# Kernel optimization log

Hardware: AMD Instinct MI355X
Metric: run time of the kernel (lower is better)

## Reference

```python
import jax, jax.numpy as jnp
import numpy as np

C = 256; HEADS = 8; LEVELS = 4; POINTS = 4; D = C // HEADS
SPATIAL = np.array([[96, 96], [48, 48], [24, 24], [12, 12]], dtype=np.int32)  # (H, W) per level
AREAS = SPATIAL[:, 0] * SPATIAL[:, 1]
HW = int(AREAS.sum())  # 12240
LSI = np.concatenate([[0], np.cumsum(AREAS)[:-1]]).astype(np.int32)
N = 1; Q = HW


def setup_inputs() -> dict:
    key = jax.random.key(0)
    ks = jax.random.split(key, 12)
    s = 0.02
    return {
        "query": jax.random.normal(ks[0], (N, Q, C), jnp.float32),
        "reference_points": jax.random.uniform(ks[1], (N, Q, LEVELS, 2), jnp.float32),
        "input_flatten": jax.random.normal(ks[2], (N, HW, C), jnp.float32),
        "input_spatial_shapes": jnp.asarray(SPATIAL),
        "input_level_start_index": jnp.asarray(LSI),
        "W_off": jax.random.normal(ks[3], (C, HEADS * LEVELS * POINTS * 2), jnp.float32) * s,
        "b_off": jax.random.normal(ks[4], (HEADS * LEVELS * POINTS * 2,), jnp.float32) * s,
        "W_attn": jax.random.normal(ks[5], (C, HEADS * LEVELS * POINTS), jnp.float32) * s,
        "b_attn": jax.random.normal(ks[6], (HEADS * LEVELS * POINTS,), jnp.float32) * s,
        "W_val": jax.random.normal(ks[7], (C, C), jnp.float32) * (1.0 / np.sqrt(C)),
        "b_val": jax.random.normal(ks[8], (C,), jnp.float32) * s,
        "W_out": jax.random.normal(ks[9], (C, C), jnp.float32) * (1.0 / np.sqrt(C)),
        "b_out": jax.random.normal(ks[10], (C,), jnp.float32) * s,
    }


def _ms_deform_attn(query, reference_points, input_flatten, sp, lsi,
                    W_off, b_off, W_attn, b_attn, W_val, b_val, W_out, b_out):
    n, q, c = query.shape
    hw = input_flatten.shape[1]
    # value projection -> [N, Hd, HW, D]
    value = (input_flatten @ W_val + b_val).reshape(n, hw, HEADS, D).transpose(0, 2, 1, 3)
    # sampling offsets [N,Q,Hd,L,P,2]
    off = (query @ W_off + b_off).reshape(n, q, HEADS, LEVELS, POINTS, 2)
    # attention weights softmaxed over L*P (done inside the fused CUDA kernel)
    attn = jax.nn.softmax((query @ W_attn + b_attn).reshape(n, q, HEADS, LEVELS * POINTS), axis=-1)
    attn = attn.reshape(n, q, HEADS, LEVELS, POINTS)
    # normalized sampling locations (reference_points last dim == 2 branch)
    norm = jnp.stack([sp[:, 1], sp[:, 0]], -1).astype(query.dtype)  # (W, H) per level
    loc = reference_points[:, :, None, :, None, :] + off / norm[None, None, None, :, None, :]
    Hl = sp[:, 0][None, None, None, :, None]
    Wl = sp[:, 1][None, None, None, :, None]
    start = lsi[None, None, None, :, None]
    # grid_sample-style (align_corners=False) pixel coordinates
    x = loc[..., 0] * Wl - 0.5
    y = loc[..., 1] * Hl - 0.5
    x0 = jnp.floor(x); y0 = jnp.floor(y)
    lx = x - x0; ly = y - y0
    x0i = x0.astype(jnp.int32); y0i = y0.astype(jnp.int32)

    def gather(yi, xi):
        valid = (xi >= 0) & (xi < Wl) & (yi >= 0) & (yi < Hl)
        idx = jnp.where(valid, start + yi * Wl + xi, 0)  # [N,Q,Hd,L,P]
        idx_t = idx.transpose(0, 2, 1, 3, 4).reshape(n, HEADS, q * LEVELS * POINTS, 1)
        g = jnp.take_along_axis(value, idx_t, axis=2)  # [N,Hd,Q*L*P,D]
        g = g.reshape(n, HEADS, q, LEVELS, POINTS, D)
        return g * valid.transpose(0, 2, 1, 3, 4)[..., None]

    def w(a):
        return a.transpose(0, 2, 1, 3, 4)[..., None]  # [N,Hd,Q,L,P,1]

    sampled = (gather(y0i, x0i) * w((1 - ly) * (1 - lx))
               + gather(y0i, x0i + 1) * w((1 - ly) * lx)
               + gather(y0i + 1, x0i) * w(ly * (1 - lx))
               + gather(y0i + 1, x0i + 1) * w(ly * lx))  # [N,Hd,Q,L,P,D]
    out = jnp.einsum('nhqlpd,nqhlp->nqhd', sampled, attn).reshape(n, q, c)
    return out @ W_out + b_out


def reference(query, reference_points, input_flatten, input_spatial_shapes, input_level_start_index,
              W_off, b_off, W_attn, b_attn, W_val, b_val, W_out, b_out):
    return _ms_deform_attn(query, reference_points, input_flatten,
                           input_spatial_shapes, input_level_start_index,
                           W_off, b_off, W_attn, b_attn, W_val, b_val, W_out, b_out)
```

## Files before the change

### kernel.cpp

```cpp
#include <hip/hip_runtime.h>

#define QTOT 12240
#define KD   256

typedef float f32x4 __attribute__((ext_vector_type(4)));
typedef short s16x8 __attribute__((ext_vector_type(8)));
typedef short s16x4 __attribute__((ext_vector_type(4)));
typedef unsigned short ushort_t;

__device__ __forceinline__ unsigned short f2b(float x) {
    union { float f; unsigned u; } c; c.f = x;
    unsigned r = c.u + 0x7fffu + ((c.u >> 16) & 1u);
    return (unsigned short)(r >> 16);
}
__device__ __forceinline__ float b2f(unsigned short u) {
    return __uint_as_float((unsigned)u << 16);
}
__device__ __forceinline__ int swz(int row, int kb) { return row * 512 + (kb ^ ((row & 7) << 4)); }

__global__ __launch_bounds__(256) void prep(
    const float* __restrict__ W_val, const float* __restrict__ W_off,
    const float* __restrict__ W_attn, const float* __restrict__ W_out,
    const float* __restrict__ b_off, const float* __restrict__ b_attn,
    ushort_t* __restrict__ WvT, ushort_t* __restrict__ WcT,
    ushort_t* __restrict__ WoT, float* __restrict__ bcomb)
{
    int id = blockIdx.x * 256 + threadIdx.x;
    if (id < 65536) { int n = id >> 8, k = id & 255; WvT[id] = f2b(W_val[k * 256 + n]); }
    else if (id < 163840) {
        int t = id - 65536; int n = t >> 8, k = t & 255;
        float v = (n < 256) ? W_off[k * 256 + n] : W_attn[k * 128 + (n - 256)];
        WcT[t] = f2b(v);
    } else if (id < 229376) {
        int t = id - 163840; int n = t >> 8, k = t & 255;
        WoT[t] = f2b(W_out[k * 256 + n]);
    } else if (id < 229760) {
        int t = id - 229376; bcomb[t] = (t < 256) ? b_off[t] : b_attn[t - 256];
    }
}

__global__ __launch_bounds__(256) void gemm1(
    const float* __restrict__ inflat, const float* __restrict__ query,
    const ushort_t* __restrict__ WvT, const ushort_t* __restrict__ WcT,
    const float* __restrict__ b_val, const float* __restrict__ bcomb,
    ushort_t* __restrict__ projb, ushort_t* __restrict__ offb,
    ushort_t* __restrict__ attnb)
{
    __shared__ char As[16384];
    const int b = blockIdx.x;
    const bool isval = b < 383;
    const int bm = (isval ? b : b - 383) * 32;
    const float* A = isval ? inflat : query;
    const ushort_t* WT = isval ? WvT : WcT;
    const int nc = isval ? 4 : 6;

    const int tid = threadIdx.x, lane = tid & 63, wave = tid >> 6;
    const int lr = lane & 15, g8 = (lane >> 4) * 8;

    {
        const float4* srcb = (const float4*)(A + (size_t)bm * KD);
        const int rem_rows = QTOT - bm;
#pragma unroll
        for (int j = 0; j < 8; ++j) {
            const int f4i = j * 256 + tid;
            const int row = f4i >> 6;
            const int colb = (f4i & 63) * 8;
            float4 f = make_float4(0.f, 0.f, 0.f, 0.f);
            if (row < rem_rows) f = srcb[f4i];
            s16x4 v;
            v[0] = f2b(f.x); v[1] = f2b(f.y); v[2] = f2b(f.z); v[3] = f2b(f.w);
            *(s16x4*)(As + swz(row, colb)) = v;
        }
    }
    __syncthreads();

    const int rg = (lane >> 4) * 4;

    for (int c = 0; c < nc; ++c) {
        const int col = c * 64 + wave * 16 + lr;
        s16x8 bfr[8];
        {
            const ushort_t* bp = WT + (size_t)col * KD + g8;
#pragma unroll
            for (int kc = 0; kc < 8; ++kc) bfr[kc] = *(const s16x8*)(bp + kc * 32);
        }
        f32x4 acc[2];
        acc[0] = (f32x4)0.f; acc[1] = (f32x4)0.f;
#pragma unroll
        for (int kc = 0; kc < 8; ++kc) {
            const int kb = (kc * 32 + g8) * 2;
            s16x8 a0 = *(const s16x8*)(As + swz(lr,      kb));
            s16x8 a1 = *(const s16x8*)(As + swz(16 + lr, kb));
            acc[0] = __builtin_amdgcn_mfma_f32_16x16x32_bf16(a0, bfr[kc], acc[0], 0, 0, 0);
            acc[1] = __builtin_amdgcn_mfma_f32_16x16x32_bf16(a1, bfr[kc], acc[1], 0, 0, 0);
        }
        const float bb = isval ? b_val[col] : bcomb[col];

        if (!isval && c >= 4) {
            const int gh = (c - 4) * 4 + wave;
            float v[2][4], m[2][4], e[2][4], s[2][4];
#pragma unroll
            for (int mf = 0; mf < 2; ++mf)
#pragma unroll
                for (int rr = 0; rr < 4; ++rr) { v[mf][rr] = acc[mf][rr] + bb; m[mf][rr] = v[mf][rr]; }
#pragma unroll
            for (int d = 1; d < 16; d <<= 1)
#pragma unroll
                for (int mf = 0; mf < 2; ++mf)
#pragma unroll
                    for (int rr = 0; rr < 4; ++rr) m[mf][rr] = fmaxf(m[mf][rr], __shfl_xor(m[mf][rr], d));
#pragma unroll
            for (int mf = 0; mf < 2; ++mf)
#pragma unroll
                for (int rr = 0; rr < 4; ++rr) { e[mf][rr] = __expf(v[mf][rr] - m[mf][rr]); s[mf][rr] = e[mf][rr]; }
#pragma unroll
            for (int d = 1; d < 16; d <<= 1)
#pragma unroll
                for (int mf = 0; mf < 2; ++mf)
#pragma unroll
                    for (int rr = 0; rr < 4; ++rr) s[mf][rr] += __shfl_xor(s[mf][rr], d);
#pragma unroll
            for (int mf = 0; mf < 2; ++mf)
#pragma unroll
                for (int rr = 0; rr < 4; ++rr) {
                    const int row = bm + mf * 16 + rg + rr;
                    if (row < QTOT)
                        attnb[(size_t)row * 128 + gh * 16 + lr] = f2b(e[mf][rr] / s[mf][rr]);
                }
        } else {
#pragma unroll
            for (int mf = 0; mf < 2; ++mf)
#pragma unroll
                for (int rr = 0; rr < 4; ++rr) {
                    const int row = bm + mf * 16 + rg + rr;
                    if (row >= QTOT) continue;
                    const float v = acc[mf][rr] + bb;
                    if (isval) projb[(size_t)row * 256 + col] = f2b(v);
                    else       offb [(size_t)row * 256 + col] = f2b(v);
                }
        }
    }
}

__global__ __launch_bounds__(256, 2) void sample7(
    const float* __restrict__ rp, const ushort_t* __restrict__ offb,
    const ushort_t* __restrict__ attnb, const ushort_t* __restrict__ projb,
    const int* __restrict__ sp, const int* __restrict__ lsi,
    ushort_t* __restrict__ outpre)
{
    const int bid = blockIdx.x;
    const int hh = (bid >= 1530) ? 1 : 0;
    const int g  = hh ? (bid - 1530) : bid;
    const int q0 = g * 8;
    const int tid = threadIdx.x;

    __shared__ int4 s_meta[512];

#pragma unroll
    for (int rep = 0; rep < 2; ++rep) {
        const int task = rep * 256 + tid;
        const int ql = task >> 6;
        const int hp = (task >> 4) & 3;
        const int lp = task & 15;
        const int l = lp >> 2;
        const int q = q0 + ql;
        const int gh = hh * 4 + hp;
        const int t128 = gh * 16 + lp;

        const float aw = b2f(attnb[(size_t)q * 128 + t128]);

        const unsigned opk = *(const unsigned*)&offb[(size_t)q * 256 + t128 * 2];
        const float ox = __uint_as_float(opk << 16);
        const float oy = __uint_as_float(opk & 0xffff0000u);

        const int Wl = 96 >> l;
        const int st = 12288 - (12288 >> (2 * l));
        const float rx = rp[((size_t)q * 4 + l) * 2 + 0];
        const float ry = rp[((size_t)q * 4 + l) * 2 + 1];

        const float x = rx * (float)Wl + ox - 0.5f;
        const float y = ry * (float)Wl + oy - 0.5f;
        const float xf = floorf(x), yf = floorf(y);
        const int x0 = (int)xf, y0 = (int)yf;
        const float lx = x - xf, ly = y - yf;

        const bool vx0 = (x0 >= 0) && (x0 < Wl);
        const bool vx1 = (x0 + 1 >= 0) && (x0 + 1 < Wl);
        const bool vy0 = (y0 >= 0) && (y0 < Wl);
        const bool vy1 = (y0 + 1 >= 0) && (y0 + 1 < Wl);

        const float w00 = (vx0 && vy0) ? aw * (1.f - ly) * (1.f - lx) : 0.f;
        const float w01 = (vx1 && vy0) ? aw * (1.f - ly) * lx         : 0.f;
        const float w10 = (vx0 && vy1) ? aw * ly * (1.f - lx)         : 0.f;
        const float w11 = (vx1 && vy1) ? aw * ly * lx                 : 0.f;
        const int i00 = (vx0 && vy0) ? st + y0 * Wl + x0           : 0;
        const int i01 = (vx1 && vy0) ? st + y0 * Wl + x0 + 1       : 0;
        const int i10 = (vx0 && vy1) ? st + (y0 + 1) * Wl + x0     : 0;
        const int i11 = (vx1 && vy1) ? st + (y0 + 1) * Wl + x0 + 1 : 0;

        int4 m;
        m.x = (i00 << 16) | (int)f2b(w00);
        m.y = (i01 << 16) | (int)f2b(w01);
        m.z = (i10 << 16) | (int)f2b(w10);
        m.w = (i11 << 16) | (int)f2b(w11);
        s_meta[task] = m;
    }
    __syncthreads();

    const int c8 = tid & 3;
    const int pq = (tid >> 2) & 1;
    const int hp = (tid >> 3) & 3;
    const int ql = tid >> 5;
    const int gh = hh * 4 + hp;
    const char* basec = (const char*)projb + (gh * 32 + c8 * 8) * 2;
    const int slot0 = (ql << 6) | (hp << 4);

    float a0 = 0, a1 = 0, a2 = 0, a3 = 0, a4 = 0, a5 = 0, a6 = 0, a7 = 0;
#pragma unroll
    for (int l = 0; l < 4; ++l) {
#pragma unroll
        for (int j = 0; j < 2; ++j) {
            const int slot = slot0 | (l << 2) | (pq * 2 + j);
            const int4 m = s_meta[slot];
#pragma unroll
            for (int c = 0; c < 4; ++c) {
                const int pk = (c == 0) ? m.x : (c == 1) ? m.y : (c == 2) ? m.z : m.w;
                const int off = (pk >> 16) << 9;
                const float w = __uint_as_float((unsigned)pk << 16);
                const uint4 v = *(const uint4*)(basec + off);
                a0 += w * __uint_as_float(v.x << 16);
                a1 += w * __uint_as_float(v.x & 0xffff0000u);
                a2 += w * __uint_as_float(v.y << 16);
                a3 += w * __uint_as_float(v.y & 0xffff0000u);
                a4 += w * __uint_as_float(v.z << 16);
                a5 += w * __uint_as_float(v.z & 0xffff0000u);
                a6 += w * __uint_as_float(v.w << 16);
                a7 += w * __uint_as_float(v.w & 0xffff0000u);
            }
        }
    }
    a0 += __shfl_xor(a0, 4); a1 += __shfl_xor(a1, 4);
    a2 += __shfl_xor(a2, 4); a3 += __shfl_xor(a3, 4);
    a4 += __shfl_xor(a4, 4); a5 += __shfl_xor(a5, 4);
    a6 += __shfl_xor(a6, 4); a7 += __shfl_xor(a7, 4);

    if (pq == 0) {
        uint4 o;
        o.x = (unsigned)f2b(a0) | ((unsigned)f2b(a1) << 16);
        o.y = (unsigned)f2b(a2) | ((unsigned)f2b(a3) << 16);
        o.z = (unsigned)f2b(a4) | ((unsigned)f2b(a5) << 16);
        o.w = (unsigned)f2b(a6) | ((unsigned)f2b(a7) << 16);
        *(uint4*)&outpre[(size_t)(q0 + ql) * 256 + gh * 32 + c8 * 8] = o;
    }
}

__global__ __launch_bounds__(256) void gemm_o(
    const ushort_t* __restrict__ Ab, const ushort_t* __restrict__ WoT,
    const float* __restrict__ b_out, float* __restrict__ out)
{
    const int bm = blockIdx.x * 32;
    const int tid = threadIdx.x, lane = tid & 63, wave = tid >> 6;
    const int lr = lane & 15, g8 = (lane >> 4) * 8;
    const int rg = (lane >> 4) * 4;

    const ushort_t* ap0;
    const ushort_t* ap1;
    {
        int r0 = bm + lr;      if (r0 >= QTOT) r0 = QTOT - 1;
        int r1 = bm + 16 + lr; if (r1 >= QTOT) r1 = QTOT - 1;
        ap0 = Ab + (size_t)r0 * KD + g8;
        ap1 = Ab + (size_t)r1 * KD + g8;
    }

#pragma unroll
    for (int c = 0; c < 4; ++c) {
        const int col = c * 64 + wave * 16 + lr;
        s16x8 bfr[8];
        {
            const ushort_t* bp = WoT + (size_t)col * KD + g8;
#pragma unroll
            for (int kc = 0; kc < 8; ++kc) bfr[kc] = *(const s16x8*)(bp + kc * 32);
        }
        f32x4 acc[2];
        acc[0] = (f32x4)0.f; acc[1] = (f32x4)0.f;
#pragma unroll
        for (int kc = 0; kc < 8; ++kc) {
            s16x8 a0 = *(const s16x8*)(ap0 + kc * 32);
            s16x8 a1 = *(const s16x8*)(ap1 + kc * 32);
            acc[0] = __builtin_amdgcn_mfma_f32_16x16x32_bf16(a0, bfr[kc], acc[0], 0, 0, 0);
            acc[1] = __builtin_amdgcn_mfma_f32_16x16x32_bf16(a1, bfr[kc], acc[1], 0, 0, 0);
        }
        const float bb = b_out[col];
#pragma unroll
        for (int mf = 0; mf < 2; ++mf)
#pragma unroll
            for (int rr = 0; rr < 4; ++rr) {
                const int row = bm + mf * 16 + rg + rr;
                if (row < QTOT) out[(size_t)row * 256 + col] = acc[mf][rr] + bb;
            }
    }
}

extern "C" void kernel_launch(void* const* d_in, const int* in_sizes, int n_in,
                              void* d_out, int out_size, void* d_ws, size_t ws_size,
                              hipStream_t stream) {
    const float* query  = (const float*)d_in[0];
    const float* rp     = (const float*)d_in[1];
    const float* inflat = (const float*)d_in[2];
    const int*   sp     = (const int*)d_in[3];
    const int*   lsi    = (const int*)d_in[4];
    const float* W_off  = (const float*)d_in[5];
    const float* b_off  = (const float*)d_in[6];
    const float* W_attn = (const float*)d_in[7];
    const float* b_attn = (const float*)d_in[8];
    const float* W_val  = (const float*)d_in[9];
    const float* b_val  = (const float*)d_in[10];
    const float* W_out  = (const float*)d_in[11];
    const float* b_out  = (const float*)d_in[12];
    float* out = (float*)d_out;

    char* ws = (char*)d_ws;
    ushort_t* projb  = (ushort_t*)ws; ws += (size_t)QTOT * 256 * 2;
    ushort_t* offb   = (ushort_t*)ws; ws += (size_t)QTOT * 256 * 2;
    ushort_t* attnb  = (ushort_t*)ws; ws += (size_t)QTOT * 128 * 2;
    ushort_t* outpre = (ushort_t*)ws; ws += (size_t)QTOT * 256 * 2;
    ushort_t* WvT    = (ushort_t*)ws; ws += 65536 * 2;
    ushort_t* WcT    = (ushort_t*)ws; ws += 98304 * 2;
    ushort_t* WoT    = (ushort_t*)ws; ws += 65536 * 2;
    float*    bcomb  = (float*)ws;    ws += 384 * 4;

    prep<<<dim3(898), dim3(256), 0, stream>>>(W_val, W_off, W_attn, W_out, b_off, b_attn,
                                              WvT, WcT, WoT, bcomb);

    gemm1<<<dim3(766), dim3(256), 0, stream>>>(inflat, query, WvT, WcT, b_val, bcomb,
                                               projb, offb, attnb);

    sample7<<<dim3(3060), dim3(256), 0, stream>>>(rp, offb, attnb, projb, sp, lsi, outpre);

    gemm_o<<<dim3(383), dim3(256), 0, stream>>>(outpre, WoT, b_out, out);
}
```

Measured before the change: 67.54 us.

## Tile weight transpose through shared memory and halve gemm1 row tile

The weight-prep kernel now transposes 32x32 tiles through shared memory, with coalesced float4 reads and vectorized bf16 writes, instead of doing strided per-element global reads. gemm1 now uses 16-row tiles, doubling the grid to 1530 blocks for better occupancy. Because 12240 divides exactly by 16, the row-bounds checks are dropped. The unused spatial-shape and level-start pointers are removed from sample7, which presumably already hardcodes them. The trade-off is that each B-fragment load in gemm1 now feeds half as many MFMAs, so weight traffic per useful flop doubles.

```diff
diff --git a/kernel.cpp b/kernel.cpp
--- a/kernel.cpp
+++ b/kernel.cpp
@@ -18,24 +18,42 @@
 }
 __device__ __forceinline__ int swz(int row, int kb) { return row * 512 + (kb ^ ((row & 7) << 4)); }
 
-__global__ __launch_bounds__(256) void prep(
+__global__ __launch_bounds__(256) void prep2(
     const float* __restrict__ W_val, const float* __restrict__ W_off,
     const float* __restrict__ W_attn, const float* __restrict__ W_out,
     const float* __restrict__ b_off, const float* __restrict__ b_attn,
     ushort_t* __restrict__ WvT, ushort_t* __restrict__ WcT,
     ushort_t* __restrict__ WoT, float* __restrict__ bcomb)
 {
-    int id = blockIdx.x * 256 + threadIdx.x;
-    if (id < 65536) { int n = id >> 8, k = id & 255; WvT[id] = f2b(W_val[k * 256 + n]); }
-    else if (id < 163840) {
-        int t = id - 65536; int n = t >> 8, k = t & 255;
-        float v = (n < 256) ? W_off[k * 256 + n] : W_attn[k * 128 + (n - 256)];
-        WcT[t] = f2b(v);
-    } else if (id < 229376) {
-        int t = id - 163840; int n = t >> 8, k = t & 255;
-        WoT[t] = f2b(W_out[k * 256 + n]);
-    } else if (id < 229760) {
-        int t = id - 229376; bcomb[t] = (t < 256) ? b_off[t] : b_attn[t - 256];
+    const int b = blockIdx.x;
+    if (b == 224) {
+        for (int t = threadIdx.x; t < 384; t += 256)
+            bcomb[t] = (t < 256) ? b_off[t] : b_attn[t - 256];
+        return;
+    }
+    __shared__ ushort_t tile[32][33];
+    const float* src; ushort_t* dst; int kt, nt, srcld, n_off;
+    if (b < 64)       { src = W_val; dst = WvT; kt = b >> 3; nt = b & 7; srcld = 256; n_off = 0; }
+    else if (b < 160) { int t = b - 64; dst = WcT; kt = t / 12; nt = t % 12;
+                        if (nt < 8) { src = W_off;  srcld = 256; n_off = 0; }
+                        else        { src = W_attn; srcld = 128; n_off = 256; } }
+    else              { int t = b - 160; src = W_out; dst = WoT; kt = t >> 3; nt = t & 7; srcld = 256; n_off = 0; }
+
+    {
+        const int r = threadIdx.x >> 3, c4 = (threadIdx.x & 7) * 4;
+        const int gk = kt * 32 + r;
+        const int gs = nt * 32 + c4 - n_off;
+        float4 f = *(const float4*)(src + (size_t)gk * srcld + gs);
+        tile[r][c4 + 0] = f2b(f.x); tile[r][c4 + 1] = f2b(f.y);
+        tile[r][c4 + 2] = f2b(f.z); tile[r][c4 + 3] = f2b(f.w);
+    }
+    __syncthreads();
+    {
+        const int r2 = threadIdx.x >> 3, k4 = (threadIdx.x & 7) * 4;
+        s16x4 v;
+        v[0] = tile[k4 + 0][r2]; v[1] = tile[k4 + 1][r2];
+        v[2] = tile[k4 + 2][r2]; v[3] = tile[k4 + 3][r2];
+        *(s16x4*)(dst + (size_t)(nt * 32 + r2) * 256 + kt * 32 + k4) = v;
     }
 }
 
@@ -46,10 +64,10 @@
     ushort_t* __restrict__ projb, ushort_t* __restrict__ offb,
     ushort_t* __restrict__ attnb)
 {
-    __shared__ char As[16384];
+    __shared__ char As[8192];
     const int b = blockIdx.x;
-    const bool isval = b < 383;
-    const int bm = (isval ? b : b - 383) * 32;
+    const bool isval = b < 765;
+    const int bm = (isval ? b : b - 765) * 16;
     const float* A = isval ? inflat : query;
     const ushort_t* WT = isval ? WvT : WcT;
     const int nc = isval ? 4 : 6;
@@ -59,14 +77,12 @@
 
     {
         const float4* srcb = (const float4*)(A + (size_t)bm * KD);
-        const int rem_rows = QTOT - bm;
-#pragma unroll
-        for (int j = 0; j < 8; ++j) {
+#pragma unroll
+        for (int j = 0; j < 4; ++j) {
             const int f4i = j * 256 + tid;
             const int row = f4i >> 6;
             const int colb = (f4i & 63) * 8;
-            float4 f = make_float4(0.f, 0.f, 0.f, 0.f);
-            if (row < rem_rows) f = srcb[f4i];
+            float4 f = srcb[f4i];
             s16x4 v;
             v[0] = f2b(f.x); v[1] = f2b(f.y); v[2] = f2b(f.z); v[3] = f2b(f.w);
             *(s16x4*)(As + swz(row, colb)) = v;
@@ -84,60 +100,40 @@
 #pragma unroll
             for (int kc = 0; kc < 8; ++kc) bfr[kc] = *(const s16x8*)(bp + kc * 32);
         }
-        f32x4 acc[2];
-        acc[0] = (f32x4)0.f; acc[1] = (f32x4)0.f;
+        f32x4 acc = (f32x4)0.f;
 #pragma unroll
         for (int kc = 0; kc < 8; ++kc) {
-            const int kb = (kc * 32 + g8) * 2;
-            s16x8 a0 = *(const s16x8*)(As + swz(lr,      kb));
-            s16x8 a1 = *(const s16x8*)(As + swz(16 + lr, kb));
-            acc[0] = __builtin_amdgcn_mfma_f32_16x16x32_bf16(a0, bfr[kc], acc[0], 0, 0, 0);
-            acc[1] = __builtin_amdgcn_mfma_f32_16x16x32_bf16(a1, bfr[kc], acc[1], 0, 0, 0);
+            s16x8 a0 = *(const s16x8*)(As + swz(lr, (kc * 32 + g8) * 2));
+            acc = __builtin_amdgcn_mfma_f32_16x16x32_bf16(a0, bfr[kc], acc, 0, 0, 0);
         }
         const float bb = isval ? b_val[col] : bcomb[col];
 
         if (!isval && c >= 4) {
             const int gh = (c - 4) * 4 + wave;
-            float v[2][4], m[2][4], e[2][4], s[2][4];
-#pragma unroll
-            for (int mf = 0; mf < 2; ++mf)
-#pragma unroll
-                for (int rr = 0; rr < 4; ++rr) { v[mf][rr] = acc[mf][rr] + bb; m[mf][rr] = v[mf][rr]; }
+            float v[4], m[4], e[4], s[4];
+#pragma unroll
+            for (int rr = 0; rr < 4; ++rr) { v[rr] = acc[rr] + bb; m[rr] = v[rr]; }
 #pragma unroll
             for (int d = 1; d < 16; d <<= 1)
 #pragma unroll
-                for (int mf = 0; mf < 2; ++mf)
-#pragma unroll
-                    for (int rr = 0; rr < 4; ++rr) m[mf][rr] = fmaxf(m[mf][rr], __shfl_xor(m[mf][rr], d));
-#pragma unroll
-            for (int mf = 0; mf < 2; ++mf)
-#pragma unroll
-                for (int rr = 0; rr < 4; ++rr) { e[mf][rr] = __expf(v[mf][rr] - m[mf][rr]); s[mf][rr] = e[mf][rr]; }
+                for (int rr = 0; rr < 4; ++rr) m[rr] = fmaxf(m[rr], __shfl_xor(m[rr], d));
+#pragma unroll
+            for (int rr = 0; rr < 4; ++rr) { e[rr] = __expf(v[rr] - m[rr]); s[rr] = e[rr]; }
 #pragma unroll
             for (int d = 1; d < 16; d <<= 1)
 #pragma unroll
-                for (int mf = 0; mf < 2; ++mf)
-#pragma unroll
-                    for (int rr = 0; rr < 4; ++rr) s[mf][rr] += __shfl_xor(s[mf][rr], d);
-#pragma unroll
-            for (int mf = 0; mf < 2; ++mf)
-#pragma unroll
-                for (int rr = 0; rr < 4; ++rr) {
-                    const int row = bm + mf * 16 + rg + rr;
-                    if (row < QTOT)
-                        attnb[(size_t)row * 128 + gh * 16 + lr] = f2b(e[mf][rr] / s[mf][rr]);
-                }
+                for (int rr = 0; rr < 4; ++rr) s[rr] += __shfl_xor(s[rr], d);
+#pragma unroll
+            for (int rr = 0; rr < 4; ++rr)
+                attnb[(size_t)(bm + rg + rr) * 128 + gh * 16 + lr] = f2b(e[rr] / s[rr]);
         } else {
 #pragma unroll
-            for (int mf = 0; mf < 2; ++mf)
-#pragma unroll
-                for (int rr = 0; rr < 4; ++rr) {
-                    const int row = bm + mf * 16 + rg + rr;
-                    if (row >= QTOT) continue;
-                    const float v = acc[mf][rr] + bb;
-                    if (isval) projb[(size_t)row * 256 + col] = f2b(v);
-                    else       offb [(size_t)row * 256 + col] = f2b(v);
-                }
+            for (int rr = 0; rr < 4; ++rr) {
+                const int row = bm + rg + rr;
+                const float v = acc[rr] + bb;
+                if (isval) projb[(size_t)row * 256 + col] = f2b(v);
+                else       offb [(size_t)row * 256 + col] = f2b(v);
+            }
         }
     }
 }
@@ -145,7 +141,6 @@
 __global__ __launch_bounds__(256, 2) void sample7(
     const float* __restrict__ rp, const ushort_t* __restrict__ offb,
     const ushort_t* __restrict__ attnb, const ushort_t* __restrict__ projb,
-    const int* __restrict__ sp, const int* __restrict__ lsi,
     ushort_t* __restrict__ outpre)
 {
     const int bid = blockIdx.x;
@@ -307,8 +302,6 @@
     const float* query  = (const float*)d_in[0];
     const float* rp     = (const float*)d_in[1];
     const float* inflat = (const float*)d_in[2];
-    const int*   sp     = (const int*)d_in[3];
-    const int*   lsi    = (const int*)d_in[4];
     const float* W_off  = (const float*)d_in[5];
     const float* b_off  = (const float*)d_in[6];
     const float* W_attn = (const float*)d_in[7];
@@ -329,13 +322,13 @@
     ushort_t* WoT    = (ushort_t*)ws; ws += 65536 * 2;
     float*    bcomb  = (float*)ws;    ws += 384 * 4;
 
-    prep<<<dim3(898), dim3(256), 0, stream>>>(W_val, W_off, W_attn, W_out, b_off, b_attn,
-                                              WvT, WcT, WoT, bcomb);
-
-    gemm1<<<dim3(766), dim3(256), 0, stream>>>(inflat, query, WvT, WcT, b_val, bcomb,
-                                               projb, offb, attnb);
-
-    sample7<<<dim3(3060), dim3(256), 0, stream>>>(rp, offb, attnb, projb, sp, lsi, outpre);
+    prep2<<<dim3(225), dim3(256), 0, stream>>>(W_val, W_off, W_attn, W_out, b_off, b_attn,
+                                               WvT, WcT, WoT, bcomb);
+
+    gemm1<<<dim3(1530), dim3(256), 0, stream>>>(inflat, query, WvT, WcT, b_val, bcomb,
+                                                projb, offb, attnb);
+
+    sample7<<<dim3(3060), dim3(256), 0, stream>>>(rp, offb, attnb, projb, outpre);
 
     gemm_o<<<dim3(383), dim3(256), 0, stream>>>(outpre, WoT, b_out, out);
 }
```

New measurement: 77.82 us. 1.15x slower.
